# Kernel tuning notes

Hardware: AMD Instinct MI355X
Metric: run time of the kernel (lower is better)

The kernel has to match this reference:

```python
import jax, jax.numpy as jnp
import numpy as np

N, IN, OUT, FAN = 4096, 4096, 4096, 64


def setup_inputs() -> dict:
    key = jax.random.key(0)
    k1, k2, k3, k4 = jax.random.split(key, 4)
    return {
        "input": jax.random.normal(k1, (N, IN), dtype=jnp.float32),
        "condensed_weight": jax.random.normal(k2, (OUT, FAN), dtype=jnp.float32) * np.float32(1.0 / np.sqrt(FAN)),
        "input_mask": jax.random.randint(k3, (OUT, FAN), 0, IN, dtype=jnp.int32),
        "bias": jax.random.normal(k4, (OUT,), dtype=jnp.float32),
    }


def reference(input, condensed_weight, input_mask, bias):
    # Fixed-fan-in sparse linear: out[b, o] = sum_k input[b, mask[o, k]] * W[o, k] + bias[o]
    # Scan over the (small, fixed) fan-in axis to avoid materializing the
    # [N, OUT, FAN] gathered tensor; each step gathers an [N, OUT] slab.
    n = input.shape[0]

    def body(acc, wk_mk):
        w_k, m_k = wk_mk            # each [OUT]
        g = jnp.take(input, m_k, axis=1)  # [N, OUT] gather of input columns
        return acc + g * w_k[None, :], None

    acc0 = jnp.zeros((n, bias.shape[0]), dtype=input.dtype) + bias[None, :]
    out, _ = jax.lax.scan(body, acc0, (condensed_weight.T, input_mask.T))
    return out
```

## Files before the change

### kernel.cpp

```cpp
#include <hip/hip_runtime.h>

#define IN_DIM   4096
#define OUT_DIM  4096
#define FAN_IN   64
#define ROWS     8
#define NTHREADS 512
#define O_PER_THREAD (OUT_DIM / NTHREADS)
#define MT_BYTES ((size_t)(FAN_IN / 4) * OUT_DIM * 16)

typedef __fp16 v2h __attribute__((ext_vector_type(2)));

__device__ __forceinline__ int bswz(int m) {
    return (m & ~7) | ((m ^ (m >> 3)) & 7);
}

__device__ __forceinline__ unsigned int pack_f16(float a, float b) {
    v2h h = __builtin_amdgcn_cvt_pkrtz(a, b);
    unsigned int u;
    __builtin_memcpy(&u, &h, sizeof(u));
    return u;
}

__global__ __launch_bounds__(256)
void schedule_mw(const int* __restrict__ M, const float* __restrict__ W,
                 int* __restrict__ Mt, float* __restrict__ Wt)
{
    const int o = blockIdx.x * 4 + (threadIdx.x >> 6);
    const int k = threadIdx.x & 63;

    const int   m    = M[(size_t)o * FAN_IN + k];
    const float w    = W[(size_t)o * FAN_IN + k];
    const int   moff = bswz(m) << 4;
    const int   g    = (moff >> 4) & 7;

    int cnt[8];
    unsigned long long same = 0;
    #pragma unroll
    for (int h = 0; h < 8; ++h) {
        const unsigned long long b = __ballot(g == h);
        cnt[h] = __popcll(b);
        if (g == h) same = b;
    }
    const unsigned long long ltmask = (k == 0) ? 0ULL : (~0ULL >> (64 - k));
    const int r = __popcll(same & ltmask);

    int slot;
    if (r < 8) {
        slot = ((g - o) & 7) + 8 * r;
    } else {
        int ovr = r - 8;
        #pragma unroll
        for (int h = 0; h < 8; ++h)
            if (h < g && cnt[h] > 8) ovr += cnt[h] - 8;
        int hstar = 0, jstar = 0, rem = ovr;
        bool found = false;
        #pragma unroll
        for (int h = 0; h < 8; ++h) {
            const int nh = (cnt[h] < 8) ? (8 - cnt[h]) : 0;
            if (!found && rem < nh) { hstar = h; jstar = cnt[h] + rem; found = true; }
            if (!found) rem -= nh;
        }
        slot = ((hstar - o) & 7) + 8 * jstar;
    }

    const int idx = ((slot >> 2) * OUT_DIM + o) * 4 + (slot & 3);
    Mt[idx] = moff;
    Wt[idx] = w;
}

#define FMAMIX_LO(acc, pk, w)                                                  \
    asm("v_fma_mix_f32 %0, %1, %2, %0 op_sel:[0,0,0] op_sel_hi:[1,0,0]"        \
        : "+v"(acc) : "v"(pk), "v"(w))
#define FMAMIX_HI(acc, pk, w)                                                  \
    asm("v_fma_mix_f32 %0, %1, %2, %0 op_sel:[1,0,0] op_sel_hi:[1,0,0]"        \
        : "+v"(acc) : "v"(pk), "v"(w))

template <bool TRANSPOSED>
__global__ __launch_bounds__(NTHREADS, 4)
void ffi_sparse_kernel(const float* __restrict__ inp,
                       const float* __restrict__ W,
                       const int*   __restrict__ M,
                       const float* __restrict__ bias,
                       const int4*  __restrict__ Mt,
                       const float4* __restrict__ Wt,
                       float* __restrict__ out)
{
    __shared__ unsigned int lds[IN_DIM * ROWS / 2];

    const int tid = threadIdx.x;
    const int r0  = blockIdx.x * ROWS;

    #pragma unroll
    for (int t = 0; t < (ROWS * IN_DIM / 16) / NTHREADS; ++t) {
        const int tile = tid + t * NTHREADS;
        const int rblk = tile >> 10;
        const int c4   = (tile & 1023) << 2;
        const float* src = inp + (size_t)(r0 + rblk * 4) * IN_DIM + c4;
        const float4 v0 = *(const float4*)(src);
        const float4 v1 = *(const float4*)(src + IN_DIM);
        const float4 v2 = *(const float4*)(src + 2 * IN_DIM);
        const float4 v3 = *(const float4*)(src + 3 * IN_DIM);

        unsigned int* p;
        p = lds + bswz(c4 + 0) * 4 + rblk * 2;
        *(uint2*)p = make_uint2(pack_f16(v0.x, v1.x), pack_f16(v2.x, v3.x));
        p = lds + bswz(c4 + 1) * 4 + rblk * 2;
        *(uint2*)p = make_uint2(pack_f16(v0.y, v1.y), pack_f16(v2.y, v3.y));
        p = lds + bswz(c4 + 2) * 4 + rblk * 2;
        *(uint2*)p = make_uint2(pack_f16(v0.z, v1.z), pack_f16(v2.z, v3.z));
        p = lds + bswz(c4 + 3) * 4 + rblk * 2;
        *(uint2*)p = make_uint2(pack_f16(v0.w, v1.w), pack_f16(v2.w, v3.w));
    }
    __syncthreads();

    const char* __restrict__ ldsb = (const char*)lds;

#define LDQ(off) (*(const uint4*)(ldsb + (off)))

#define CONSUME(d, wv) {                                                       \
        FMAMIX_LO(acc0, d.x, wv);  FMAMIX_HI(acc1, d.x, wv);                   \
        FMAMIX_LO(acc2, d.y, wv);  FMAMIX_HI(acc3, d.y, wv);                   \
        FMAMIX_LO(acc4, d.z, wv);  FMAMIX_HI(acc5, d.z, wv);                   \
        FMAMIX_LO(acc6, d.w, wv);  FMAMIX_HI(acc7, d.w, wv);                   \
    }
#define ISSUE4(D0,D1,D2,D3, MN) {                                              \
        D0 = LDQ(MN.x); D1 = LDQ(MN.y); D2 = LDQ(MN.z); D3 = LDQ(MN.w); }
#define CONS4(D0,D1,D2,D3, WC) {                                               \
        CONSUME(D0, WC.x); CONSUME(D1, WC.y);                                  \
        CONSUME(D2, WC.z); CONSUME(D3, WC.w); }
#define MWLD(dm, dw, idx) {                                                    \
        if (TRANSPOSED) {                                                      \
            dm = Mt[(idx) * OUT_DIM + o];                                      \
            dw = Wt[(idx) * OUT_DIM + o];                                      \
        } else {                                                               \
            int4 mr = mp[(idx)];                                               \
            mr.x = bswz(mr.x) << 4; mr.y = bswz(mr.y) << 4;                    \
            mr.z = bswz(mr.z) << 4; mr.w = bswz(mr.w) << 4;                    \
            dm = mr; dw = wp[(idx)];                                           \
        } }

    #pragma unroll 1
    for (int i = 0; i < O_PER_THREAD; ++i) {
        const int o = tid + i * NTHREADS;
        const float bv = bias[o];
        float acc0 = bv, acc1 = bv, acc2 = bv, acc3 = bv;
        float acc4 = bv, acc5 = bv, acc6 = bv, acc7 = bv;

        const int4*   mp = (const int4*)(M + (size_t)o * FAN_IN);
        const float4* wp = (const float4*)(W + (size_t)o * FAN_IN);

        int4   m0, m1, m2, m3;
        float4 w0, w1, w2, w3;
        uint4  dA0, dA1, dA2, dA3, dB0, dB1, dB2, dB3;

        MWLD(m0, w0, 0);  MWLD(m1, w1, 1);  MWLD(m2, w2, 2);
        ISSUE4(dA0,dA1,dA2,dA3, m0);

        ISSUE4(dB0,dB1,dB2,dB3, m1);  MWLD(m3,w3, 3);   CONS4(dA0,dA1,dA2,dA3, w0);
        ISSUE4(dA0,dA1,dA2,dA3, m2);  MWLD(m0,w0, 4);   CONS4(dB0,dB1,dB2,dB3, w1);
        ISSUE4(dB0,dB1,dB2,dB3, m3);  MWLD(m1,w1, 5);   CONS4(dA0,dA1,dA2,dA3, w2);
        ISSUE4(dA0,dA1,dA2,dA3, m0);  MWLD(m2,w2, 6);   CONS4(dB0,dB1,dB2,dB3, w3);
        ISSUE4(dB0,dB1,dB2,dB3, m1);  MWLD(m3,w3, 7);   CONS4(dA0,dA1,dA2,dA3, w0);
        ISSUE4(dA0,dA1,dA2,dA3, m2);  MWLD(m0,w0, 8);   CONS4(dB0,dB1,dB2,dB3, w1);
        ISSUE4(dB0,dB1,dB2,dB3, m3);  MWLD(m1,w1, 9);   CONS4(dA0,dA1,dA2,dA3, w2);
        ISSUE4(dA0,dA1,dA2,dA3, m0);  MWLD(m2,w2,10);   CONS4(dB0,dB1,dB2,dB3, w3);
        ISSUE4(dB0,dB1,dB2,dB3, m1);  MWLD(m3,w3,11);   CONS4(dA0,dA1,dA2,dA3, w0);
        ISSUE4(dA0,dA1,dA2,dA3, m2);  MWLD(m0,w0,12);   CONS4(dB0,dB1,dB2,dB3, w1);
        ISSUE4(dB0,dB1,dB2,dB3, m3);  MWLD(m1,w1,13);   CONS4(dA0,dA1,dA2,dA3, w2);
        ISSUE4(dA0,dA1,dA2,dA3, m0);  MWLD(m2,w2,14);   CONS4(dB0,dB1,dB2,dB3, w3);
        ISSUE4(dB0,dB1,dB2,dB3, m1);  MWLD(m3,w3,15);   CONS4(dA0,dA1,dA2,dA3, w0);
        ISSUE4(dA0,dA1,dA2,dA3, m2);                    CONS4(dB0,dB1,dB2,dB3, w1);
        ISSUE4(dB0,dB1,dB2,dB3, m3);                    CONS4(dA0,dA1,dA2,dA3, w2);
                                                        CONS4(dB0,dB1,dB2,dB3, w3);

        float* op = out + (size_t)r0 * OUT_DIM + o;
        op[0 * OUT_DIM] = acc0;
        op[1 * OUT_DIM] = acc1;
        op[2 * OUT_DIM] = acc2;
        op[3 * OUT_DIM] = acc3;
        op[4 * OUT_DIM] = acc4;
        op[5 * OUT_DIM] = acc5;
        op[6 * OUT_DIM] = acc6;
        op[7 * OUT_DIM] = acc7;
    }
#undef CONSUME
#undef ISSUE4
#undef CONS4
#undef MWLD
#undef LDQ
}

extern "C" void kernel_launch(void* const* d_in, const int* in_sizes, int n_in,
                              void* d_out, int out_size, void* d_ws, size_t ws_size,
                              hipStream_t stream) {
    const float* inp  = (const float*)d_in[0];
    const float* W    = (const float*)d_in[1];
    const int*   M    = (const int*)d_in[2];
    const float* bias = (const float*)d_in[3];
    float* out = (float*)d_out;

    const int n_rows = in_sizes[0] / IN_DIM;
    dim3 grid(n_rows / ROWS), block(NTHREADS);

    const bool use_t = ws_size >= 2 * MT_BYTES;
    if (use_t) {
        int*   Mt = (int*)d_ws;
        float* Wt = (float*)((char*)d_ws + MT_BYTES);
        schedule_mw<<<dim3(OUT_DIM / 4), dim3(256), 0, stream>>>(M, W, Mt, Wt);
        ffi_sparse_kernel<true><<<grid, block, 0, stream>>>(inp, W, M, bias,
                                                            (const int4*)Mt,
                                                            (const float4*)Wt, out);
    } else {
        ffi_sparse_kernel<false><<<grid, block, 0, stream>>>(inp, W, M, bias,
                                                             (const int4*)nullptr,
                                                             (const float4*)nullptr, out);
    }
}
```

Baseline: 71.99 us.

## Halve rows per block, pack indices as u16 and weights as fp16

Rows per block drop from 8 to 4, so the LDS tile halves and launch bounds request 8 blocks per CU instead of 4 for higher occupancy. The precomputed index and weight schedule is packed as 16-bit offsets and fp16 weights, halving that traffic, and the FMA-mix ops read the fp16 weight from the lo or hi half. The cost is reloading the index and weight stream for twice as many blocks, one LDS gather yielding only 4 rows, and lower weight precision.

New measurement: 97.42 us. 35.3% more time.

```diff
diff --git a/kernel.cpp b/kernel.cpp
--- a/kernel.cpp
+++ b/kernel.cpp
@@ -3,10 +3,10 @@
 #define IN_DIM   4096
 #define OUT_DIM  4096
 #define FAN_IN   64
-#define ROWS     8
+#define ROWS     4
 #define NTHREADS 512
 #define O_PER_THREAD (OUT_DIM / NTHREADS)
-#define MT_BYTES ((size_t)(FAN_IN / 4) * OUT_DIM * 16)
+#define MT_BYTES ((size_t)(FAN_IN / 4) * OUT_DIM * 8)
 
 typedef __fp16 v2h __attribute__((ext_vector_type(2)));
 
@@ -23,15 +23,15 @@
 
 __global__ __launch_bounds__(256)
 void schedule_mw(const int* __restrict__ M, const float* __restrict__ W,
-                 int* __restrict__ Mt, float* __restrict__ Wt)
+                 unsigned short* __restrict__ Mt, __fp16* __restrict__ Wt)
 {
     const int o = blockIdx.x * 4 + (threadIdx.x >> 6);
     const int k = threadIdx.x & 63;
 
     const int   m    = M[(size_t)o * FAN_IN + k];
     const float w    = W[(size_t)o * FAN_IN + k];
-    const int   moff = bswz(m) << 4;
-    const int   g    = (moff >> 4) & 7;
+    const int   mb   = bswz(m);
+    const int   g    = mb & 7;
 
     int cnt[8];
     unsigned long long same = 0;
@@ -64,25 +64,31 @@
     }
 
     const int idx = ((slot >> 2) * OUT_DIM + o) * 4 + (slot & 3);
-    Mt[idx] = moff;
-    Wt[idx] = w;
-}
-
-#define FMAMIX_LO(acc, pk, w)                                                  \
-    asm("v_fma_mix_f32 %0, %1, %2, %0 op_sel:[0,0,0] op_sel_hi:[1,0,0]"        \
-        : "+v"(acc) : "v"(pk), "v"(w))
-#define FMAMIX_HI(acc, pk, w)                                                  \
-    asm("v_fma_mix_f32 %0, %1, %2, %0 op_sel:[1,0,0] op_sel_hi:[1,0,0]"        \
-        : "+v"(acc) : "v"(pk), "v"(w))
+    Mt[idx] = (unsigned short)(mb << 3);
+    Wt[idx] = (__fp16)w;
+}
+
+#define FMIX_LL(acc, pk, wp)                                                   \
+    asm("v_fma_mix_f32 %0, %1, %2, %0 op_sel:[0,0,0] op_sel_hi:[1,1,0]"        \
+        : "+v"(acc) : "v"(pk), "v"(wp))
+#define FMIX_HL(acc, pk, wp)                                                   \
+    asm("v_fma_mix_f32 %0, %1, %2, %0 op_sel:[1,0,0] op_sel_hi:[1,1,0]"        \
+        : "+v"(acc) : "v"(pk), "v"(wp))
+#define FMIX_LH(acc, pk, wp)                                                   \
+    asm("v_fma_mix_f32 %0, %1, %2, %0 op_sel:[0,1,0] op_sel_hi:[1,1,0]"        \
+        : "+v"(acc) : "v"(pk), "v"(wp))
+#define FMIX_HH(acc, pk, wp)                                                   \
+    asm("v_fma_mix_f32 %0, %1, %2, %0 op_sel:[1,1,0] op_sel_hi:[1,1,0]"        \
+        : "+v"(acc) : "v"(pk), "v"(wp))
 
 template <bool TRANSPOSED>
-__global__ __launch_bounds__(NTHREADS, 4)
+__global__ __launch_bounds__(NTHREADS, 8)
 void ffi_sparse_kernel(const float* __restrict__ inp,
                        const float* __restrict__ W,
                        const int*   __restrict__ M,
                        const float* __restrict__ bias,
-                       const int4*  __restrict__ Mt,
-                       const float4* __restrict__ Wt,
+                       const uint2* __restrict__ Mt,
+                       const uint2* __restrict__ Wt,
                        float* __restrict__ out)
 {
     __shared__ unsigned int lds[IN_DIM * ROWS / 2];
@@ -91,52 +97,49 @@
     const int r0  = blockIdx.x * ROWS;
 
     #pragma unroll
-    for (int t = 0; t < (ROWS * IN_DIM / 16) / NTHREADS; ++t) {
+    for (int t = 0; t < 2; ++t) {
         const int tile = tid + t * NTHREADS;
-        const int rblk = tile >> 10;
-        const int c4   = (tile & 1023) << 2;
-        const float* src = inp + (size_t)(r0 + rblk * 4) * IN_DIM + c4;
+        const int c4   = tile << 2;
+        const float* src = inp + (size_t)r0 * IN_DIM + c4;
         const float4 v0 = *(const float4*)(src);
         const float4 v1 = *(const float4*)(src + IN_DIM);
         const float4 v2 = *(const float4*)(src + 2 * IN_DIM);
         const float4 v3 = *(const float4*)(src + 3 * IN_DIM);
 
-        unsigned int* p;
-        p = lds + bswz(c4 + 0) * 4 + rblk * 2;
-        *(uint2*)p = make_uint2(pack_f16(v0.x, v1.x), pack_f16(v2.x, v3.x));
-        p = lds + bswz(c4 + 1) * 4 + rblk * 2;
-        *(uint2*)p = make_uint2(pack_f16(v0.y, v1.y), pack_f16(v2.y, v3.y));
-        p = lds + bswz(c4 + 2) * 4 + rblk * 2;
-        *(uint2*)p = make_uint2(pack_f16(v0.z, v1.z), pack_f16(v2.z, v3.z));
-        p = lds + bswz(c4 + 3) * 4 + rblk * 2;
-        *(uint2*)p = make_uint2(pack_f16(v0.w, v1.w), pack_f16(v2.w, v3.w));
+        uint2* lds2 = (uint2*)lds;
+        lds2[bswz(c4 + 0)] = make_uint2(pack_f16(v0.x, v1.x), pack_f16(v2.x, v3.x));
+        lds2[bswz(c4 + 1)] = make_uint2(pack_f16(v0.y, v1.y), pack_f16(v2.y, v3.y));
+        lds2[bswz(c4 + 2)] = make_uint2(pack_f16(v0.z, v1.z), pack_f16(v2.z, v3.z));
+        lds2[bswz(c4 + 3)] = make_uint2(pack_f16(v0.w, v1.w), pack_f16(v2.w, v3.w));
     }
     __syncthreads();
 
     const char* __restrict__ ldsb = (const char*)lds;
 
-#define LDQ(off) (*(const uint4*)(ldsb + (off)))
-
-#define CONSUME(d, wv) {                                                       \
-        FMAMIX_LO(acc0, d.x, wv);  FMAMIX_HI(acc1, d.x, wv);                   \
-        FMAMIX_LO(acc2, d.y, wv);  FMAMIX_HI(acc3, d.y, wv);                   \
-        FMAMIX_LO(acc4, d.z, wv);  FMAMIX_HI(acc5, d.z, wv);                   \
-        FMAMIX_LO(acc6, d.w, wv);  FMAMIX_HI(acc7, d.w, wv);                   \
-    }
+#define LD64(off) (*(const uint2*)(ldsb + (off)))
+
+#define CONSUME_WL(D, WP) {                                                    \
+        FMIX_LL(acc0, D.x, WP);  FMIX_HL(acc1, D.x, WP);                       \
+        FMIX_LL(acc2, D.y, WP);  FMIX_HL(acc3, D.y, WP); }
+#define CONSUME_WH(D, WP) {                                                    \
+        FMIX_LH(acc0, D.x, WP);  FMIX_HH(acc1, D.x, WP);                       \
+        FMIX_LH(acc2, D.y, WP);  FMIX_HH(acc3, D.y, WP); }
 #define ISSUE4(D0,D1,D2,D3, MN) {                                              \
-        D0 = LDQ(MN.x); D1 = LDQ(MN.y); D2 = LDQ(MN.z); D3 = LDQ(MN.w); }
+        D0 = LD64(MN.x & 0xFFFFu); D1 = LD64(MN.x >> 16);                      \
+        D2 = LD64(MN.y & 0xFFFFu); D3 = LD64(MN.y >> 16); }
 #define CONS4(D0,D1,D2,D3, WC) {                                               \
-        CONSUME(D0, WC.x); CONSUME(D1, WC.y);                                  \
-        CONSUME(D2, WC.z); CONSUME(D3, WC.w); }
+        CONSUME_WL(D0, WC.x); CONSUME_WH(D1, WC.x);                            \
+        CONSUME_WL(D2, WC.y); CONSUME_WH(D3, WC.y); }
 #define MWLD(dm, dw, idx) {                                                    \
         if (TRANSPOSED) {                                                      \
             dm = Mt[(idx) * OUT_DIM + o];                                      \
             dw = Wt[(idx) * OUT_DIM + o];                                      \
         } else {                                                               \
             int4 mr = mp[(idx)];                                               \
-            mr.x = bswz(mr.x) << 4; mr.y = bswz(mr.y) << 4;                    \
-            mr.z = bswz(mr.z) << 4; mr.w = bswz(mr.w) << 4;                    \
-            dm = mr; dw = wp[(idx)];                                           \
+            dm.x = (unsigned)(bswz(mr.x) << 3) | ((unsigned)(bswz(mr.y) << 3) << 16); \
+            dm.y = (unsigned)(bswz(mr.z) << 3) | ((unsigned)(bswz(mr.w) << 3) << 16); \
+            float4 wr = wp[(idx)];                                             \
+            dw.x = pack_f16(wr.x, wr.y); dw.y = pack_f16(wr.z, wr.w);          \
         } }
 
     #pragma unroll 1
@@ -144,14 +147,13 @@
         const int o = tid + i * NTHREADS;
         const float bv = bias[o];
         float acc0 = bv, acc1 = bv, acc2 = bv, acc3 = bv;
-        float acc4 = bv, acc5 = bv, acc6 = bv, acc7 = bv;
 
         const int4*   mp = (const int4*)(M + (size_t)o * FAN_IN);
         const float4* wp = (const float4*)(W + (size_t)o * FAN_IN);
 
-        int4   m0, m1, m2, m3;
-        float4 w0, w1, w2, w3;
-        uint4  dA0, dA1, dA2, dA3, dB0, dB1, dB2, dB3;
+        uint2  m0, m1, m2, m3;
+        uint2  w0, w1, w2, w3;
+        uint2  dA0, dA1, dA2, dA3, dB0, dB1, dB2, dB3;
 
         MWLD(m0, w0, 0);  MWLD(m1, w1, 1);  MWLD(m2, w2, 2);
         ISSUE4(dA0,dA1,dA2,dA3, m0);
@@ -178,16 +180,13 @@
         op[1 * OUT_DIM] = acc1;
         op[2 * OUT_DIM] = acc2;
         op[3 * OUT_DIM] = acc3;
-        op[4 * OUT_DIM] = acc4;
-        op[5 * OUT_DIM] = acc5;
-        op[6 * OUT_DIM] = acc6;
-        op[7 * OUT_DIM] = acc7;
-    }
-#undef CONSUME
+    }
+#undef CONSUME_WL
+#undef CONSUME_WH
 #undef ISSUE4
 #undef CONS4
 #undef MWLD
-#undef LDQ
+#undef LD64
 }
 
 extern "C" void kernel_launch(void* const* d_in, const int* in_sizes, int n_in,
@@ -204,15 +203,15 @@
 
     const bool use_t = ws_size >= 2 * MT_BYTES;
     if (use_t) {
-        int*   Mt = (int*)d_ws;
-        float* Wt = (float*)((char*)d_ws + MT_BYTES);
+        unsigned short* Mt = (unsigned short*)d_ws;
+        __fp16*         Wt = (__fp16*)((char*)d_ws + MT_BYTES);
         schedule_mw<<<dim3(OUT_DIM / 4), dim3(256), 0, stream>>>(M, W, Mt, Wt);
         ffi_sparse_kernel<true><<<grid, block, 0, stream>>>(inp, W, M, bias,
-                                                            (const int4*)Mt,
-                                                            (const float4*)Wt, out);
+                                                            (const uint2*)Mt,
+                                                            (const uint2*)Wt, out);
     } else {
         ffi_sparse_kernel<false><<<grid, block, 0, stream>>>(inp, W, M, bias,
-                                                             (const int4*)nullptr,
-                                                             (const float4*)nullptr, out);
-    }
-}
+                                                             (const uint2*)nullptr,
+                                                             (const uint2*)nullptr, out);
+    }
+}
```

## Process two row tiles per block, prefetching the second during the first

Applied to the files above, without the earlier changes.

Each block now handles two 8-row tiles with 1024 threads and double-buffered LDS. Global loads for the second tile are issued into registers before the first tile's compute and written to the second LDS buffer afterwards. This is meant to hide input-load latency behind compute and halve the number of blocks. In exchange, LDS per block doubles to 128KB, which limits occupancy to one block per CU, and register pressure rises from the held prefetch values under launch_bounds(1024,4).

New measurement: 88.51 us. 22.9% more time.

```diff
diff --git a/kernel.cpp b/kernel.cpp
--- a/kernel.cpp
+++ b/kernel.cpp
@@ -4,8 +4,8 @@
 #define OUT_DIM  4096
 #define FAN_IN   64
 #define ROWS     8
-#define NTHREADS 512
-#define O_PER_THREAD (OUT_DIM / NTHREADS)
+#define NTHREADS 1024
+#define OPT      (OUT_DIM / NTHREADS)
 #define MT_BYTES ((size_t)(FAN_IN / 4) * OUT_DIM * 16)
 
 typedef __fp16 v2h __attribute__((ext_vector_type(2)));
@@ -76,47 +76,14 @@
         : "+v"(acc) : "v"(pk), "v"(w))
 
 template <bool TRANSPOSED>
-__global__ __launch_bounds__(NTHREADS, 4)
-void ffi_sparse_kernel(const float* __restrict__ inp,
-                       const float* __restrict__ W,
-                       const int*   __restrict__ M,
-                       const float* __restrict__ bias,
-                       const int4*  __restrict__ Mt,
-                       const float4* __restrict__ Wt,
-                       float* __restrict__ out)
+__device__ __forceinline__ void compute_tile(
+    const char* __restrict__ ldsb,
+    const int4* __restrict__ Mt, const float4* __restrict__ Wt,
+    const float* __restrict__ W, const int* __restrict__ M,
+    const float* __restrict__ bias, float* __restrict__ out,
+    int r0, int tid)
 {
-    __shared__ unsigned int lds[IN_DIM * ROWS / 2];
-
-    const int tid = threadIdx.x;
-    const int r0  = blockIdx.x * ROWS;
-
-    #pragma unroll
-    for (int t = 0; t < (ROWS * IN_DIM / 16) / NTHREADS; ++t) {
-        const int tile = tid + t * NTHREADS;
-        const int rblk = tile >> 10;
-        const int c4   = (tile & 1023) << 2;
-        const float* src = inp + (size_t)(r0 + rblk * 4) * IN_DIM + c4;
-        const float4 v0 = *(const float4*)(src);
-        const float4 v1 = *(const float4*)(src + IN_DIM);
-        const float4 v2 = *(const float4*)(src + 2 * IN_DIM);
-        const float4 v3 = *(const float4*)(src + 3 * IN_DIM);
-
-        unsigned int* p;
-        p = lds + bswz(c4 + 0) * 4 + rblk * 2;
-        *(uint2*)p = make_uint2(pack_f16(v0.x, v1.x), pack_f16(v2.x, v3.x));
-        p = lds + bswz(c4 + 1) * 4 + rblk * 2;
-        *(uint2*)p = make_uint2(pack_f16(v0.y, v1.y), pack_f16(v2.y, v3.y));
-        p = lds + bswz(c4 + 2) * 4 + rblk * 2;
-        *(uint2*)p = make_uint2(pack_f16(v0.z, v1.z), pack_f16(v2.z, v3.z));
-        p = lds + bswz(c4 + 3) * 4 + rblk * 2;
-        *(uint2*)p = make_uint2(pack_f16(v0.w, v1.w), pack_f16(v2.w, v3.w));
-    }
-    __syncthreads();
-
-    const char* __restrict__ ldsb = (const char*)lds;
-
 #define LDQ(off) (*(const uint4*)(ldsb + (off)))
-
 #define CONSUME(d, wv) {                                                       \
         FMAMIX_LO(acc0, d.x, wv);  FMAMIX_HI(acc1, d.x, wv);                   \
         FMAMIX_LO(acc2, d.y, wv);  FMAMIX_HI(acc3, d.y, wv);                   \
@@ -140,7 +107,7 @@
         } }
 
     #pragma unroll 1
-    for (int i = 0; i < O_PER_THREAD; ++i) {
+    for (int i = 0; i < OPT; ++i) {
         const int o = tid + i * NTHREADS;
         const float bv = bias[o];
         float acc0 = bv, acc1 = bv, acc2 = bv, acc3 = bv;
@@ -190,6 +157,80 @@
 #undef LDQ
 }
 
+template <bool TRANSPOSED>
+__global__ __launch_bounds__(NTHREADS, 4)
+void ffi_sparse_kernel(const float* __restrict__ inp,
+                       const float* __restrict__ W,
+                       const int*   __restrict__ M,
+                       const float* __restrict__ bias,
+                       const int4*  __restrict__ Mt,
+                       const float4* __restrict__ Wt,
+                       float* __restrict__ out)
+{
+    __shared__ unsigned int lds[2][IN_DIM * ROWS / 2];
+
+    const int tid = threadIdx.x;
+    const int r0a = blockIdx.x * ROWS;
+    const int r0b = (blockIdx.x + gridDim.x) * ROWS;
+    const int c4  = tid << 2;
+
+    #pragma unroll
+    for (int t = 0; t < 2; ++t) {
+        const float* src = inp + (size_t)(r0a + t * 4) * IN_DIM + c4;
+        const float4 v0 = *(const float4*)(src);
+        const float4 v1 = *(const float4*)(src + IN_DIM);
+        const float4 v2 = *(const float4*)(src + 2 * IN_DIM);
+        const float4 v3 = *(const float4*)(src + 3 * IN_DIM);
+        unsigned int* p;
+        p = &lds[0][0] + bswz(c4 + 0) * 4 + t * 2;
+        *(uint2*)p = make_uint2(pack_f16(v0.x, v1.x), pack_f16(v2.x, v3.x));
+        p = &lds[0][0] + bswz(c4 + 1) * 4 + t * 2;
+        *(uint2*)p = make_uint2(pack_f16(v0.y, v1.y), pack_f16(v2.y, v3.y));
+        p = &lds[0][0] + bswz(c4 + 2) * 4 + t * 2;
+        *(uint2*)p = make_uint2(pack_f16(v0.z, v1.z), pack_f16(v2.z, v3.z));
+        p = &lds[0][0] + bswz(c4 + 3) * 4 + t * 2;
+        *(uint2*)p = make_uint2(pack_f16(v0.w, v1.w), pack_f16(v2.w, v3.w));
+    }
+    __syncthreads();
+
+    const float* sB0 = inp + (size_t)(r0b) * IN_DIM + c4;
+    const float* sB1 = inp + (size_t)(r0b + 4) * IN_DIM + c4;
+    const float4 qa0 = *(const float4*)(sB0);
+    const float4 qa1 = *(const float4*)(sB0 + IN_DIM);
+    const float4 qa2 = *(const float4*)(sB0 + 2 * IN_DIM);
+    const float4 qa3 = *(const float4*)(sB0 + 3 * IN_DIM);
+    const float4 qb0 = *(const float4*)(sB1);
+    const float4 qb1 = *(const float4*)(sB1 + IN_DIM);
+    const float4 qb2 = *(const float4*)(sB1 + 2 * IN_DIM);
+    const float4 qb3 = *(const float4*)(sB1 + 3 * IN_DIM);
+
+    compute_tile<TRANSPOSED>((const char*)&lds[0][0], Mt, Wt, W, M, bias, out, r0a, tid);
+
+    {
+        unsigned int* b1 = &lds[1][0];
+        unsigned int* p;
+        p = b1 + bswz(c4 + 0) * 4;
+        *(uint2*)p = make_uint2(pack_f16(qa0.x, qa1.x), pack_f16(qa2.x, qa3.x));
+        p = b1 + bswz(c4 + 1) * 4;
+        *(uint2*)p = make_uint2(pack_f16(qa0.y, qa1.y), pack_f16(qa2.y, qa3.y));
+        p = b1 + bswz(c4 + 2) * 4;
+        *(uint2*)p = make_uint2(pack_f16(qa0.z, qa1.z), pack_f16(qa2.z, qa3.z));
+        p = b1 + bswz(c4 + 3) * 4;
+        *(uint2*)p = make_uint2(pack_f16(qa0.w, qa1.w), pack_f16(qa2.w, qa3.w));
+        p = b1 + bswz(c4 + 0) * 4 + 2;
+        *(uint2*)p = make_uint2(pack_f16(qb0.x, qb1.x), pack_f16(qb2.x, qb3.x));
+        p = b1 + bswz(c4 + 1) * 4 + 2;
+        *(uint2*)p = make_uint2(pack_f16(qb0.y, qb1.y), pack_f16(qb2.y, qb3.y));
+        p = b1 + bswz(c4 + 2) * 4 + 2;
+        *(uint2*)p = make_uint2(pack_f16(qb0.z, qb1.z), pack_f16(qb2.z, qb3.z));
+        p = b1 + bswz(c4 + 3) * 4 + 2;
+        *(uint2*)p = make_uint2(pack_f16(qb0.w, qb1.w), pack_f16(qb2.w, qb3.w));
+    }
+    __syncthreads();
+
+    compute_tile<TRANSPOSED>((const char*)&lds[1][0], Mt, Wt, W, M, bias, out, r0b, tid);
+}
+
 extern "C" void kernel_launch(void* const* d_in, const int* in_sizes, int n_in,
                               void* d_out, int out_size, void* d_ws, size_t ws_size,
                               hipStream_t stream) {
@@ -200,7 +241,7 @@
     float* out = (float*)d_out;
 
     const int n_rows = in_sizes[0] / IN_DIM;
-    dim3 grid(n_rows / ROWS), block(NTHREADS);
+    dim3 grid(n_rows / (ROWS * 2)), block(NTHREADS);
 
     const bool use_t = ws_size >= 2 * MT_BYTES;
     if (use_t) {
```
